# Performance work log

Hardware: AMD Instinct MI355X
Metric: run time of the kernel (lower is better)

Reference implementation:

```python
import jax, jax.numpy as jnp
import numpy as np

P = 512       # input_shape
HD = 256      # hidden_dim
N = 65536     # number of samples
LAM1 = 1.0
LAM3 = 1.0


def setup_inputs() -> dict:
    key = jax.random.key(0)
    ks = jax.random.split(key, 12)
    def lin(kw, kb, out_d, in_d):
        lim = 1.0 / np.sqrt(in_d)
        W = jax.random.uniform(kw, (out_d, in_d), jnp.float32, -lim, lim)
        b = jax.random.uniform(kb, (out_d,), jnp.float32, -lim, lim)
        return W, b
    W1, b1 = lin(ks[0], ks[1], 200, P + HD)
    W12, b12 = lin(ks[2], ks[3], 100, 200)
    W13, b13 = lin(ks[4], ks[5], 100, 100)
    W2, b2 = lin(ks[6], ks[7], P, 100)
    return {
        "input": jax.random.normal(ks[8], (N, P), jnp.float32),
        "h": jax.random.normal(ks[9], (N, HD), jnp.float32),
        "W1": W1, "b1": b1, "W12": W12, "b12": b12,
        "W13": W13, "b13": b13, "W2": W2, "b2": b2,
        "idx0": 0, "idx1": N,
    }


def reference(input, h, W1, b1, W12, b12, W13, b13, W2, b2, idx0, idx1):
    n = input.shape[0]
    hs = h[idx0:idx1]                                   # [N, HD]
    x = jnp.concatenate([input, hs], axis=1)            # [N, P+HD]
    x = jax.nn.relu(x @ W1.T + b1)                      # dropout = identity (eval)
    x = jax.nn.relu(x @ W12.T + b12)
    x = jax.nn.relu(x @ W13.T + b13)
    f_x_h = x @ W2.T + b2                               # [N, P]
    mu = jnp.mean(hs, axis=0)                           # [HD]
    # S = mean_i <h_i, h_i> : vectorized sum-of-squares (replaces Python loop)
    S = jnp.mean(jnp.sum(hs * hs, axis=1))
    part0 = jnp.linalg.norm(f_x_h[:-1] - input[1:]) / (n - 1)
    part1 = LAM1 * jnp.sum(jnp.abs(mu)) / HD
    part2 = LAM1 * jnp.abs(S / HD - 1.0)
    part3 = LAM3 * jnp.mean(jnp.sum(jnp.abs(hs[1:] - hs[:-1]), axis=1)) / HD
    return (f_x_h, part0, part1, part2, part3)
```

## Files before the change

### kernel.cpp

```cpp
#include <hip/hip_runtime.h>

typedef __bf16 bf16;
typedef __bf16 bf16x4 __attribute__((ext_vector_type(4)));
typedef __bf16 bf16x8 __attribute__((ext_vector_type(8)));
typedef float f32x4 __attribute__((ext_vector_type(4)));

#define N_ROWS 65536

#define W1_E   159744
#define W12_E  25088
#define W13_E  14336
#define W2_E   65536
#define WP_TOTAL (W1_E + W12_E + W13_E + W2_E)
#define W12_OFF_B 319488
#define W13_OFF_B 369664
#define W2_OFF_B  398336
#define BP_OFF_BYTES (WP_TOTAL * 2)
#define BP_FLOATS 944
#define ACC_OFF_BYTES (BP_OFF_BYTES + BP_FLOATS * 4)
#define NCOPY 16
#define P0_IDX (NCOPY * 256)
#define S_IDX0 (P0_IDX + 1)
#define P3_IDX0 (S_IDX0 + NCOPY)
#define ACC_FLOATS (P3_IDX0 + NCOPY)

__device__ inline int swz4(int r) { return (r ^ (r >> 2)) & 3; }

__global__ void pack_kernel(const float* __restrict__ W1, const float* __restrict__ b1,
                            const float* __restrict__ W12, const float* __restrict__ b12,
                            const float* __restrict__ W13, const float* __restrict__ b13,
                            const float* __restrict__ W2, const float* __restrict__ b2,
                            bf16* __restrict__ wp, float* __restrict__ bp) {
  int i = blockIdx.x * 256 + threadIdx.x;
  if (i < WP_TOTAL) {
    float v = 0.0f;
    if (i < W1_E) {
      int s = i / 6656, b = i - s * 6656;
      int r = b >> 5, w = b & 31;
      int k = s * 32 + (((w >> 3) ^ swz4(r)) << 3) + (w & 7);
      if (r < 200) v = W1[r * 768 + k];
    } else if (i < W1_E + W12_E) {
      int j = i - W1_E;
      int s = j / 3584, b = j - s * 3584;
      int r = b >> 5, w = b & 31;
      int k = s * 32 + (((w >> 3) ^ swz4(r)) << 3) + (w & 7);
      if (r < 100 && k < 200) v = W12[r * 200 + k];
    } else if (i < W1_E + W12_E + W13_E) {
      int j = i - (W1_E + W12_E);
      int s = j / 3584, b = j - s * 3584;
      int r = b >> 5, w = b & 31;
      int k = s * 32 + (((w >> 3) ^ swz4(r)) << 3) + (w & 7);
      if (r < 100 && k < 100) v = W13[r * 100 + k];
    } else {
      int j = i - (W1_E + W12_E + W13_E);
      int g = j >> 14, rest = j & 16383;
      int s = rest >> 12, b = rest & 4095;
      int r = b >> 5, w = b & 31;
      int o = g * 128 + r;
      int k = s * 32 + (((w >> 3) ^ swz4(r)) << 3) + (w & 7);
      if (k < 100) v = W2[o * 100 + k];
    }
    wp[i] = (bf16)v;
  } else {
    int j = i - WP_TOTAL;
    if (j < BP_FLOATS) {
      float v = 0.0f;
      if (j < 208)      { if (j < 200) v = b1[j]; }
      else if (j < 320) { int o = j - 208; if (o < 100) v = b12[o]; }
      else if (j < 432) { int o = j - 320; if (o < 100) v = b13[o]; }
      else              { v = b2[j - 432]; }
      bp[j] = v;
    }
  }
}

#define MFMA(a, b, c) __builtin_amdgcn_mfma_f32_16x16x32_bf16((a), (b), (c), 0, 0, 0)

template<int BYTES>
__device__ inline void stage(const char* __restrict__ src, bf16* __restrict__ dstw, int tid) {
  char* dst = (char*)dstw;
  const int off0 = (tid >> 6) * 1024 + (tid & 63) * 16;
  constexpr int NCH = (BYTES + 4095) / 4096;
#pragma unroll
  for (int j = 0; j < NCH; j++) {
    const int off = j * 4096 + off0;
    if ((BYTES & 4095) == 0 || off < BYTES)
      __builtin_amdgcn_global_load_lds(
          (const __attribute__((address_space(1))) void*)(src + off),
          (__attribute__((address_space(3))) void*)(dst + off),
          16, 0, 0);
  }
}

__global__ __launch_bounds__(256, 2) void mlp_main(
    const float* __restrict__ input, const float* __restrict__ h,
    const bf16* __restrict__ wp, const float* __restrict__ bp,
    float* __restrict__ out, float* __restrict__ acc) {
  __shared__ __align__(16) bf16 acts[4][3712];
  __shared__ __align__(16) bf16 wbuf[2][6656];
  __shared__ float wred[4][3];

  const int tid = threadIdx.x;
  const int lane = tid & 63;
  const int wave = tid >> 6;
  const int c16 = lane & 15;
  const int quad = lane >> 4;
  const int m0 = blockIdx.x * 64 + wave * 16;
  const int qs8 = (quad ^ swz4(c16)) * 8;

  const char* wpb = (const char*)wp;
  const float* b1p  = bp;
  const float* b12p = bp + 208;
  const float* b13p = bp + 320;
  const float* b2p  = bp + 432;

  bf16* actw = &acts[wave][0];
  bf16* aw = actw;

  f32x4 csA = (f32x4){0.f, 0.f, 0.f, 0.f};
  f32x4 csB = (f32x4){0.f, 0.f, 0.f, 0.f};
  float s2loc = 0.0f, p3loc = 0.0f;

  f32x4 acc1[13];
#pragma unroll
  for (int t = 0; t < 13; t++) acc1[t] = (f32x4){0.f, 0.f, 0.f, 0.f};

  f32x4 ar[8];
  auto loadA = [&](int kb) {
#pragma unroll
    for (int i = 0; i < 8; i++) {
      const int row = 2 * i + (lane >> 5);
      const int col = (lane & 31) * 4;
      const float* src = (kb < 4)
          ? (input + (size_t)(m0 + row) * 512 + kb * 128 + col)
          : (h + (size_t)(m0 + row) * 256 + (kb - 4) * 128 + col);
      ar[i] = *(const f32x4*)src;
    }
  };
  auto writeA = [&]() {
    const int kk = (lane & 31) >> 3;
    const int q  = ((lane & 31) >> 1) & 3;
    const int sub = (lane & 1) * 4;
#pragma unroll
    for (int i = 0; i < 8; i++) {
      const int row = 2 * i + (lane >> 5);
      bf16x4 cv;
#pragma unroll
      for (int c = 0; c < 4; c++) cv[c] = (bf16)ar[i][c];
      *(bf16x4*)(aw + kk * 512 + row * 32 + ((q ^ swz4(row)) * 8) + sub) = cv;
    }
  };

  stage<13312>(wpb, wbuf[0], tid);
  loadA(0);

  for (int kb = 0; kb < 6; kb++) {
    writeA();
    if (kb >= 4) {
      f32x4* cs = (kb == 4) ? &csA : &csB;
#pragma unroll
      for (int i = 0; i < 8; i++) {
        f32x4 oth;
#pragma unroll
        for (int c = 0; c < 4; c++) oth[c] = __shfl_xor(ar[i][c], 32);
        *cs += ar[i];
#pragma unroll
        for (int c = 0; c < 4; c++) s2loc += ar[i][c] * ar[i][c];
        if (lane < 32) {
#pragma unroll
          for (int c = 0; c < 4; c++) p3loc += __builtin_fabsf(oth[c] - ar[i][c]);
        } else if (i >= 1) {
#pragma unroll
          for (int c = 0; c < 4; c++) p3loc += __builtin_fabsf(oth[c] - ar[i - 1][c]);
        }
      }
    }
    __syncthreads();
#pragma unroll
    for (int j = 0; j < 4; j++) {
      const int ks = kb * 4 + j;
      if (j == 0 && kb + 1 < 6) loadA(kb + 1);
      if (ks + 1 < 24) stage<13312>(wpb + (ks + 1) * 13312, wbuf[(ks + 1) & 1], tid);
      bf16x8 a = *(const bf16x8*)(aw + j * 512 + c16 * 32 + qs8);
      const bf16* buf = wbuf[ks & 1];
#pragma unroll
      for (int t = 0; t < 13; t++) {
        bf16x8 bb = *(const bf16x8*)(buf + (t * 16 + c16) * 32 + qs8);
        acc1[t] = MFMA(a, bb, acc1[t]);
      }
      __syncthreads();
    }
  }
#pragma unroll
  for (int t = 0; t < 13; t++) {
    const float bias = b1p[t * 16 + c16];
#pragma unroll
    for (int r = 0; r < 4; r++)
      actw[(quad * 4 + r) * 232 + t * 16 + c16] = (bf16)fmaxf(acc1[t][r] + bias, 0.0f);
  }
  for (int idx = lane; idx < 256; idx += 64)
    actw[(idx >> 4) * 232 + 208 + (idx & 15)] = (bf16)0.0f;

  f32x4 acc2[7];
#pragma unroll
  for (int t = 0; t < 7; t++) acc2[t] = (f32x4){0.f, 0.f, 0.f, 0.f};

  stage<7168>(wpb + W12_OFF_B, wbuf[0], tid);
  __syncthreads();
#pragma unroll
  for (int ks = 0; ks < 7; ks++) {
    if (ks + 1 < 7) stage<7168>(wpb + W12_OFF_B + (ks + 1) * 7168, wbuf[(ks + 1) & 1], tid);
    bf16x8 a = *(const bf16x8*)(actw + c16 * 232 + ks * 32 + quad * 8);
    const bf16* buf = wbuf[ks & 1];
#pragma unroll
    for (int t = 0; t < 7; t++) {
      bf16x8 bb = *(const bf16x8*)(buf + (t * 16 + c16) * 32 + qs8);
      acc2[t] = MFMA(a, bb, acc2[t]);
    }
    __syncthreads();
  }
#pragma unroll
  for (int t = 0; t < 7; t++) {
    const float bias = b12p[t * 16 + c16];
#pragma unroll
    for (int r = 0; r < 4; r++)
      actw[(quad * 4 + r) * 136 + t * 16 + c16] = (bf16)fmaxf(acc2[t][r] + bias, 0.0f);
  }
  for (int idx = lane; idx < 256; idx += 64)
    actw[(idx >> 4) * 136 + 112 + (idx & 15)] = (bf16)0.0f;

  f32x4 acc3[7];
#pragma unroll
  for (int t = 0; t < 7; t++) acc3[t] = (f32x4){0.f, 0.f, 0.f, 0.f};

  stage<7168>(wpb + W13_OFF_B, wbuf[0], tid);
  __syncthreads();
#pragma unroll
  for (int ks = 0; ks < 4; ks++) {
    if (ks + 1 < 4) stage<7168>(wpb + W13_OFF_B + (ks + 1) * 7168, wbuf[(ks + 1) & 1], tid);
    bf16x8 a = *(const bf16x8*)(actw + c16 * 136 + ks * 32 + quad * 8);
    const bf16* buf = wbuf[ks & 1];
#pragma unroll
    for (int t = 0; t < 7; t++) {
      bf16x8 bb = *(const bf16x8*)(buf + (t * 16 + c16) * 32 + qs8);
      acc3[t] = MFMA(a, bb, acc3[t]);
    }
    __syncthreads();
  }
#pragma unroll
  for (int t = 0; t < 7; t++) {
    const float bias = b13p[t * 16 + c16];
#pragma unroll
    for (int r = 0; r < 4; r++)
      actw[(quad * 4 + r) * 136 + t * 16 + c16] = (bf16)fmaxf(acc3[t][r] + bias, 0.0f);
  }
  for (int idx = lane; idx < 256; idx += 64)
    actw[(idx >> 4) * 136 + 112 + (idx & 15)] = (bf16)0.0f;

  float p0local = 0.0f;
  for (int g = 0; g < 4; g++) {
    f32x4 acc4[8];
#pragma unroll
    for (int t = 0; t < 8; t++) acc4[t] = (f32x4){0.f, 0.f, 0.f, 0.f};

    const char* Wg = wpb + W2_OFF_B + g * 32768;
    stage<8192>(Wg, wbuf[0], tid);
    __syncthreads();
#pragma unroll
    for (int ks = 0; ks < 4; ks++) {
      if (ks + 1 < 4) stage<8192>(Wg + (ks + 1) * 8192, wbuf[(ks + 1) & 1], tid);
      bf16x8 a = *(const bf16x8*)(actw + c16 * 136 + ks * 32 + quad * 8);
      const bf16* buf = wbuf[ks & 1];
#pragma unroll
      for (int t = 0; t < 8; t++) {
        bf16x8 bb = *(const bf16x8*)(buf + (t * 16 + c16) * 32 + qs8);
        acc4[t] = MFMA(a, bb, acc4[t]);
      }
      __syncthreads();
    }
#pragma unroll
    for (int t = 0; t < 8; t++) {
      const int o = g * 128 + t * 16 + c16;
      const float bias = b2p[o];
#pragma unroll
      for (int r = 0; r < 4; r++) {
        const int grow = m0 + quad * 4 + r;
        float v = acc4[t][r] + bias;
        out[(size_t)grow * 512 + o] = v;
        if (grow < N_ROWS - 1) {
          float d = v - input[(size_t)(grow + 1) * 512 + o];
          p0local += d * d;
        }
      }
    }
  }

  {
    const int p = tid >> 6, cq = tid & 63;
    const int rowA = blockIdx.x * 64 + p * 16 + 15;
    if (rowA + 1 < N_ROWS) {
      f32x4 a = *(const f32x4*)(h + (size_t)rowA * 256 + cq * 4);
      f32x4 b = *(const f32x4*)(h + (size_t)(rowA + 1) * 256 + cq * 4);
#pragma unroll
      for (int c = 0; c < 4; c++) p3loc += __builtin_fabsf(b[c] - a[c]);
    }
  }
#pragma unroll
  for (int c = 0; c < 4; c++) {
    csA[c] += __shfl_xor(csA[c], 32);
    csB[c] += __shfl_xor(csB[c], 32);
  }
  f32x4* hred = (f32x4*)&acts[0][0];
  if (lane < 32) hred[wave * 64 + lane] = csA;
  else           hred[wave * 64 + 32 + (lane & 31)] = csB;
#pragma unroll
  for (int off = 32; off > 0; off >>= 1) {
    p0local += __shfl_down(p0local, off);
    s2loc   += __shfl_down(s2loc, off);
    p3loc   += __shfl_down(p3loc, off);
  }
  if (lane == 0) { wred[wave][0] = p0local; wred[wave][1] = s2loc; wred[wave][2] = p3loc; }
  __syncthreads();
  if (tid < 64) {
    f32x4 tot = hred[tid] + hred[64 + tid] + hred[128 + tid] + hred[192 + tid];
    float* dst = acc + (blockIdx.x & (NCOPY - 1)) * 256 + tid * 4;
    atomicAdd(dst + 0, tot[0]);
    atomicAdd(dst + 1, tot[1]);
    atomicAdd(dst + 2, tot[2]);
    atomicAdd(dst + 3, tot[3]);
  }
  if (tid == 0) {
    atomicAdd(&acc[P0_IDX], wred[0][0] + wred[1][0] + wred[2][0] + wred[3][0]);
    atomicAdd(&acc[S_IDX0 + (blockIdx.x & (NCOPY - 1))], wred[0][1] + wred[1][1] + wred[2][1] + wred[3][1]);
    atomicAdd(&acc[P3_IDX0 + (blockIdx.x & (NCOPY - 1))], wred[0][2] + wred[1][2] + wred[2][2] + wred[3][2]);
  }
}

__global__ void finalize(const float* __restrict__ acc, float* __restrict__ out) {
  __shared__ float red[256];
  const int t = threadIdx.x;
  float s = 0.0f;
#pragma unroll
  for (int j = 0; j < NCOPY; j++) s += acc[j * 256 + t];
  red[t] = fabsf(s);
  __syncthreads();
  for (int st = 128; st > 0; st >>= 1) {
    if (t < st) red[t] += red[t + st];
    __syncthreads();
  }
  if (t == 0) {
    float Ssum = 0.f, Psum = 0.f;
#pragma unroll
    for (int j = 0; j < NCOPY; j++) { Ssum += acc[S_IDX0 + j]; Psum += acc[P3_IDX0 + j]; }
    out[(size_t)N_ROWS * 512 + 0] = sqrtf(acc[P0_IDX]) / 65535.0f;
    out[(size_t)N_ROWS * 512 + 1] = red[0] / 65536.0f / 256.0f;
    out[(size_t)N_ROWS * 512 + 2] = fabsf(Ssum / (65536.0f * 256.0f) - 1.0f);
    out[(size_t)N_ROWS * 512 + 3] = Psum / (65535.0f * 256.0f);
  }
}

extern "C" void kernel_launch(void* const* d_in, const int* in_sizes, int n_in,
                              void* d_out, int out_size, void* d_ws, size_t ws_size,
                              hipStream_t stream) {
  const float* input = (const float*)d_in[0];
  const float* h   = (const float*)d_in[1];
  const float* W1  = (const float*)d_in[2];
  const float* b1  = (const float*)d_in[3];
  const float* W12 = (const float*)d_in[4];
  const float* b12 = (const float*)d_in[5];
  const float* W13 = (const float*)d_in[6];
  const float* b13 = (const float*)d_in[7];
  const float* W2  = (const float*)d_in[8];
  const float* b2  = (const float*)d_in[9];
  float* out = (float*)d_out;

  bf16* wp = (bf16*)d_ws;
  float* bp = (float*)((char*)d_ws + BP_OFF_BYTES);
  float* acc = (float*)((char*)d_ws + ACC_OFF_BYTES);

  hipMemsetAsync(acc, 0, ACC_FLOATS * sizeof(float), stream);
  pack_kernel<<<(WP_TOTAL + BP_FLOATS + 255) / 256, 256, 0, stream>>>(
      W1, b1, W12, b12, W13, b13, W2, b2, wp, bp);
  mlp_main<<<N_ROWS / 64, 256, 0, stream>>>(input, h, wp, bp, out, acc);
  finalize<<<1, 256, 0, stream>>>(acc, out);
}
```

Baseline: 408.5 us.

## Process two 64-row tiles per block to reuse layer-1 weight stages

Each block now handles 128 rows as two 64-row sets, running layer-1 MFMAs for both against each staged W1 slice, so W1 LDS staging is amortized over twice the rows and the grid is halved. Layer-1 A operands are now loaded straight from global fp32 and converted in registers instead of going through the LDS swizzle buffer. The h statistics are computed in interleaved steps, and layers 2-4 run sequentially per row set. This raises register pressure (two sets of 13 accumulators) under launch bounds of 2 blocks per CU, and the direct global A loads may be less coalesced.

```diff
diff --git a/kernel.cpp b/kernel.cpp
--- a/kernel.cpp
+++ b/kernel.cpp
@@ -76,6 +76,15 @@
 
 #define MFMA(a, b, c) __builtin_amdgcn_mfma_f32_16x16x32_bf16((a), (b), (c), 0, 0, 0)
 
+__device__ inline bf16x8 cvt8(const float* __restrict__ p) {
+  f32x4 lo = *(const f32x4*)p;
+  f32x4 hi = *(const f32x4*)(p + 4);
+  bf16x8 r;
+#pragma unroll
+  for (int i = 0; i < 4; i++) { r[i] = (bf16)lo[i]; r[4 + i] = (bf16)hi[i]; }
+  return r;
+}
+
 template<int BYTES>
 __device__ inline void stage(const char* __restrict__ src, bf16* __restrict__ dstw, int tid) {
   char* dst = (char*)dstw;
@@ -105,7 +114,8 @@
   const int wave = tid >> 6;
   const int c16 = lane & 15;
   const int quad = lane >> 4;
-  const int m0 = blockIdx.x * 64 + wave * 16;
+  const int m0A = blockIdx.x * 128 + wave * 16;
+  const int m0B = m0A + 64;
   const int qs8 = (quad ^ swz4(c16)) * 8;
 
   const char* wpb = (const char*)wp;
@@ -115,194 +125,195 @@
   const float* b2p  = bp + 432;
 
   bf16* actw = &acts[wave][0];
-  bf16* aw = actw;
 
   f32x4 csA = (f32x4){0.f, 0.f, 0.f, 0.f};
   f32x4 csB = (f32x4){0.f, 0.f, 0.f, 0.f};
   float s2loc = 0.0f, p3loc = 0.0f;
-
-  f32x4 acc1[13];
-#pragma unroll
-  for (int t = 0; t < 13; t++) acc1[t] = (f32x4){0.f, 0.f, 0.f, 0.f};
+  float p0local = 0.0f;
 
   f32x4 ar[8];
-  auto loadA = [&](int kb) {
+  auto loadH = [&](int base, int half) {
 #pragma unroll
     for (int i = 0; i < 8; i++) {
       const int row = 2 * i + (lane >> 5);
-      const int col = (lane & 31) * 4;
-      const float* src = (kb < 4)
-          ? (input + (size_t)(m0 + row) * 512 + kb * 128 + col)
-          : (h + (size_t)(m0 + row) * 256 + (kb - 4) * 128 + col);
-      ar[i] = *(const f32x4*)src;
+      ar[i] = *(const f32x4*)(h + (size_t)(base + row) * 256 + half * 128 + (lane & 31) * 4);
     }
   };
-  auto writeA = [&]() {
-    const int kk = (lane & 31) >> 3;
-    const int q  = ((lane & 31) >> 1) & 3;
-    const int sub = (lane & 1) * 4;
+  auto statsH = [&](f32x4* cs) {
 #pragma unroll
     for (int i = 0; i < 8; i++) {
-      const int row = 2 * i + (lane >> 5);
-      bf16x4 cv;
-#pragma unroll
-      for (int c = 0; c < 4; c++) cv[c] = (bf16)ar[i][c];
-      *(bf16x4*)(aw + kk * 512 + row * 32 + ((q ^ swz4(row)) * 8) + sub) = cv;
+      f32x4 oth;
+#pragma unroll
+      for (int c = 0; c < 4; c++) oth[c] = __shfl_xor(ar[i][c], 32);
+      *cs += ar[i];
+#pragma unroll
+      for (int c = 0; c < 4; c++) s2loc += ar[i][c] * ar[i][c];
+      if (lane < 32) {
+#pragma unroll
+        for (int c = 0; c < 4; c++) p3loc += __builtin_fabsf(oth[c] - ar[i][c]);
+      } else if (i >= 1) {
+#pragma unroll
+        for (int c = 0; c < 4; c++) p3loc += __builtin_fabsf(oth[c] - ar[i - 1][c]);
+      }
     }
   };
 
+  f32x4 accA[13], accB[13];
+#pragma unroll
+  for (int t = 0; t < 13; t++) {
+    accA[t] = (f32x4){0.f, 0.f, 0.f, 0.f};
+    accB[t] = (f32x4){0.f, 0.f, 0.f, 0.f};
+  }
+
   stage<13312>(wpb, wbuf[0], tid);
-  loadA(0);
-
-  for (int kb = 0; kb < 6; kb++) {
-    writeA();
-    if (kb >= 4) {
-      f32x4* cs = (kb == 4) ? &csA : &csB;
-#pragma unroll
-      for (int i = 0; i < 8; i++) {
-        f32x4 oth;
-#pragma unroll
-        for (int c = 0; c < 4; c++) oth[c] = __shfl_xor(ar[i][c], 32);
-        *cs += ar[i];
-#pragma unroll
-        for (int c = 0; c < 4; c++) s2loc += ar[i][c] * ar[i][c];
-        if (lane < 32) {
-#pragma unroll
-          for (int c = 0; c < 4; c++) p3loc += __builtin_fabsf(oth[c] - ar[i][c]);
-        } else if (i >= 1) {
-#pragma unroll
-          for (int c = 0; c < 4; c++) p3loc += __builtin_fabsf(oth[c] - ar[i - 1][c]);
-        }
-      }
+  __syncthreads();
+
+  const float* aArow = input + (size_t)(m0A + c16) * 512 + quad * 8;
+  const float* aBrow = input + (size_t)(m0B + c16) * 512 + quad * 8;
+  const float* hArow = h + (size_t)(m0A + c16) * 256 + quad * 8;
+  const float* hBrow = h + (size_t)(m0B + c16) * 256 + quad * 8;
+
+  for (int ks = 0; ks < 24; ks++) {
+    if (ks + 1 < 24) stage<13312>(wpb + (ks + 1) * 13312, wbuf[(ks + 1) & 1], tid);
+    if (ks == 15) loadH(m0A, 0);
+    else if (ks == 16) statsH(&csA);
+    else if (ks == 17) loadH(m0A, 1);
+    else if (ks == 18) statsH(&csB);
+    else if (ks == 19) loadH(m0B, 0);
+    else if (ks == 20) statsH(&csA);
+    else if (ks == 21) loadH(m0B, 1);
+    else if (ks == 22) statsH(&csB);
+    const int k0 = ks * 32;
+    bf16x8 aA = (k0 < 512) ? cvt8(aArow + k0) : cvt8(hArow + (k0 - 512));
+    bf16x8 aB = (k0 < 512) ? cvt8(aBrow + k0) : cvt8(hBrow + (k0 - 512));
+    const bf16* buf = wbuf[ks & 1];
+#pragma unroll
+    for (int t = 0; t < 13; t++) {
+      bf16x8 bb = *(const bf16x8*)(buf + (t * 16 + c16) * 32 + qs8);
+      accA[t] = MFMA(aA, bb, accA[t]);
+      accB[t] = MFMA(aB, bb, accB[t]);
     }
     __syncthreads();
-#pragma unroll
-    for (int j = 0; j < 4; j++) {
-      const int ks = kb * 4 + j;
-      if (j == 0 && kb + 1 < 6) loadA(kb + 1);
-      if (ks + 1 < 24) stage<13312>(wpb + (ks + 1) * 13312, wbuf[(ks + 1) & 1], tid);
-      bf16x8 a = *(const bf16x8*)(aw + j * 512 + c16 * 32 + qs8);
+  }
+
+  auto runL234 = [&](f32x4 (&acc1)[13], int m0) {
+#pragma unroll
+    for (int t = 0; t < 13; t++) {
+      const float bias = b1p[t * 16 + c16];
+#pragma unroll
+      for (int r = 0; r < 4; r++)
+        actw[(quad * 4 + r) * 232 + t * 16 + c16] = (bf16)fmaxf(acc1[t][r] + bias, 0.0f);
+    }
+    for (int idx = lane; idx < 256; idx += 64)
+      actw[(idx >> 4) * 232 + 208 + (idx & 15)] = (bf16)0.0f;
+
+    f32x4 acc2[7];
+#pragma unroll
+    for (int t = 0; t < 7; t++) acc2[t] = (f32x4){0.f, 0.f, 0.f, 0.f};
+    stage<7168>(wpb + W12_OFF_B, wbuf[0], tid);
+    __syncthreads();
+#pragma unroll
+    for (int ks = 0; ks < 7; ks++) {
+      if (ks + 1 < 7) stage<7168>(wpb + W12_OFF_B + (ks + 1) * 7168, wbuf[(ks + 1) & 1], tid);
+      bf16x8 a = *(const bf16x8*)(actw + c16 * 232 + ks * 32 + quad * 8);
       const bf16* buf = wbuf[ks & 1];
 #pragma unroll
-      for (int t = 0; t < 13; t++) {
+      for (int t = 0; t < 7; t++) {
         bf16x8 bb = *(const bf16x8*)(buf + (t * 16 + c16) * 32 + qs8);
-        acc1[t] = MFMA(a, bb, acc1[t]);
+        acc2[t] = MFMA(a, bb, acc2[t]);
       }
       __syncthreads();
     }
-  }
-#pragma unroll
-  for (int t = 0; t < 13; t++) {
-    const float bias = b1p[t * 16 + c16];
-#pragma unroll
-    for (int r = 0; r < 4; r++)
-      actw[(quad * 4 + r) * 232 + t * 16 + c16] = (bf16)fmaxf(acc1[t][r] + bias, 0.0f);
-  }
-  for (int idx = lane; idx < 256; idx += 64)
-    actw[(idx >> 4) * 232 + 208 + (idx & 15)] = (bf16)0.0f;
-
-  f32x4 acc2[7];
-#pragma unroll
-  for (int t = 0; t < 7; t++) acc2[t] = (f32x4){0.f, 0.f, 0.f, 0.f};
-
-  stage<7168>(wpb + W12_OFF_B, wbuf[0], tid);
-  __syncthreads();
-#pragma unroll
-  for (int ks = 0; ks < 7; ks++) {
-    if (ks + 1 < 7) stage<7168>(wpb + W12_OFF_B + (ks + 1) * 7168, wbuf[(ks + 1) & 1], tid);
-    bf16x8 a = *(const bf16x8*)(actw + c16 * 232 + ks * 32 + quad * 8);
-    const bf16* buf = wbuf[ks & 1];
 #pragma unroll
     for (int t = 0; t < 7; t++) {
-      bf16x8 bb = *(const bf16x8*)(buf + (t * 16 + c16) * 32 + qs8);
-      acc2[t] = MFMA(a, bb, acc2[t]);
-    }
+      const float bias = b12p[t * 16 + c16];
+#pragma unroll
+      for (int r = 0; r < 4; r++)
+        actw[(quad * 4 + r) * 136 + t * 16 + c16] = (bf16)fmaxf(acc2[t][r] + bias, 0.0f);
+    }
+    for (int idx = lane; idx < 256; idx += 64)
+      actw[(idx >> 4) * 136 + 112 + (idx & 15)] = (bf16)0.0f;
+
+    f32x4 acc3[7];
+#pragma unroll
+    for (int t = 0; t < 7; t++) acc3[t] = (f32x4){0.f, 0.f, 0.f, 0.f};
+    stage<7168>(wpb + W13_OFF_B, wbuf[0], tid);
     __syncthreads();
-  }
-#pragma unroll
-  for (int t = 0; t < 7; t++) {
-    const float bias = b12p[t * 16 + c16];
-#pragma unroll
-    for (int r = 0; r < 4; r++)
-      actw[(quad * 4 + r) * 136 + t * 16 + c16] = (bf16)fmaxf(acc2[t][r] + bias, 0.0f);
-  }
-  for (int idx = lane; idx < 256; idx += 64)
-    actw[(idx >> 4) * 136 + 112 + (idx & 15)] = (bf16)0.0f;
-
-  f32x4 acc3[7];
-#pragma unroll
-  for (int t = 0; t < 7; t++) acc3[t] = (f32x4){0.f, 0.f, 0.f, 0.f};
-
-  stage<7168>(wpb + W13_OFF_B, wbuf[0], tid);
-  __syncthreads();
-#pragma unroll
-  for (int ks = 0; ks < 4; ks++) {
-    if (ks + 1 < 4) stage<7168>(wpb + W13_OFF_B + (ks + 1) * 7168, wbuf[(ks + 1) & 1], tid);
-    bf16x8 a = *(const bf16x8*)(actw + c16 * 136 + ks * 32 + quad * 8);
-    const bf16* buf = wbuf[ks & 1];
-#pragma unroll
-    for (int t = 0; t < 7; t++) {
-      bf16x8 bb = *(const bf16x8*)(buf + (t * 16 + c16) * 32 + qs8);
-      acc3[t] = MFMA(a, bb, acc3[t]);
-    }
-    __syncthreads();
-  }
-#pragma unroll
-  for (int t = 0; t < 7; t++) {
-    const float bias = b13p[t * 16 + c16];
-#pragma unroll
-    for (int r = 0; r < 4; r++)
-      actw[(quad * 4 + r) * 136 + t * 16 + c16] = (bf16)fmaxf(acc3[t][r] + bias, 0.0f);
-  }
-  for (int idx = lane; idx < 256; idx += 64)
-    actw[(idx >> 4) * 136 + 112 + (idx & 15)] = (bf16)0.0f;
-
-  float p0local = 0.0f;
-  for (int g = 0; g < 4; g++) {
-    f32x4 acc4[8];
-#pragma unroll
-    for (int t = 0; t < 8; t++) acc4[t] = (f32x4){0.f, 0.f, 0.f, 0.f};
-
-    const char* Wg = wpb + W2_OFF_B + g * 32768;
-    stage<8192>(Wg, wbuf[0], tid);
-    __syncthreads();
 #pragma unroll
     for (int ks = 0; ks < 4; ks++) {
-      if (ks + 1 < 4) stage<8192>(Wg + (ks + 1) * 8192, wbuf[(ks + 1) & 1], tid);
+      if (ks + 1 < 4) stage<7168>(wpb + W13_OFF_B + (ks + 1) * 7168, wbuf[(ks + 1) & 1], tid);
       bf16x8 a = *(const bf16x8*)(actw + c16 * 136 + ks * 32 + quad * 8);
       const bf16* buf = wbuf[ks & 1];
 #pragma unroll
+      for (int t = 0; t < 7; t++) {
+        bf16x8 bb = *(const bf16x8*)(buf + (t * 16 + c16) * 32 + qs8);
+        acc3[t] = MFMA(a, bb, acc3[t]);
+      }
+      __syncthreads();
+    }
+#pragma unroll
+    for (int t = 0; t < 7; t++) {
+      const float bias = b13p[t * 16 + c16];
+#pragma unroll
+      for (int r = 0; r < 4; r++)
+        actw[(quad * 4 + r) * 136 + t * 16 + c16] = (bf16)fmaxf(acc3[t][r] + bias, 0.0f);
+    }
+    for (int idx = lane; idx < 256; idx += 64)
+      actw[(idx >> 4) * 136 + 112 + (idx & 15)] = (bf16)0.0f;
+
+    for (int g = 0; g < 4; g++) {
+      f32x4 acc4[8];
+#pragma unroll
+      for (int t = 0; t < 8; t++) acc4[t] = (f32x4){0.f, 0.f, 0.f, 0.f};
+      const char* Wg = wpb + W2_OFF_B + g * 32768;
+      stage<8192>(Wg, wbuf[0], tid);
+      __syncthreads();
+#pragma unroll
+      for (int ks = 0; ks < 4; ks++) {
+        if (ks + 1 < 4) stage<8192>(Wg + (ks + 1) * 8192, wbuf[(ks + 1) & 1], tid);
+        bf16x8 a = *(const bf16x8*)(actw + c16 * 136 + ks * 32 + quad * 8);
+        const bf16* buf = wbuf[ks & 1];
+#pragma unroll
+        for (int t = 0; t < 8; t++) {
+          bf16x8 bb = *(const bf16x8*)(buf + (t * 16 + c16) * 32 + qs8);
+          acc4[t] = MFMA(a, bb, acc4[t]);
+        }
+        __syncthreads();
+      }
+#pragma unroll
       for (int t = 0; t < 8; t++) {
-        bf16x8 bb = *(const bf16x8*)(buf + (t * 16 + c16) * 32 + qs8);
-        acc4[t] = MFMA(a, bb, acc4[t]);
-      }
-      __syncthreads();
-    }
-#pragma unroll
-    for (int t = 0; t < 8; t++) {
-      const int o = g * 128 + t * 16 + c16;
-      const float bias = b2p[o];
-#pragma unroll
-      for (int r = 0; r < 4; r++) {
-        const int grow = m0 + quad * 4 + r;
-        float v = acc4[t][r] + bias;
-        out[(size_t)grow * 512 + o] = v;
-        if (grow < N_ROWS - 1) {
-          float d = v - input[(size_t)(grow + 1) * 512 + o];
-          p0local += d * d;
+        const int o = g * 128 + t * 16 + c16;
+        const float bias = b2p[o];
+#pragma unroll
+        for (int r = 0; r < 4; r++) {
+          const int grow = m0 + quad * 4 + r;
+          float v = acc4[t][r] + bias;
+          out[(size_t)grow * 512 + o] = v;
+          if (grow < N_ROWS - 1) {
+            float d = v - input[(size_t)(grow + 1) * 512 + o];
+            p0local += d * d;
+          }
         }
       }
     }
-  }
+  };
+
+  runL234(accA, m0A);
+  runL234(accB, m0B);
 
   {
-    const int p = tid >> 6, cq = tid & 63;
-    const int rowA = blockIdx.x * 64 + p * 16 + 15;
+    const int g = tid >> 5, cq = tid & 31;
+    const int rowA = blockIdx.x * 128 + g * 16 + 15;
     if (rowA + 1 < N_ROWS) {
-      f32x4 a = *(const f32x4*)(h + (size_t)rowA * 256 + cq * 4);
-      f32x4 b = *(const f32x4*)(h + (size_t)(rowA + 1) * 256 + cq * 4);
-#pragma unroll
-      for (int c = 0; c < 4; c++) p3loc += __builtin_fabsf(b[c] - a[c]);
+      f32x4 a0 = *(const f32x4*)(h + (size_t)rowA * 256 + cq * 8);
+      f32x4 a1 = *(const f32x4*)(h + (size_t)rowA * 256 + cq * 8 + 4);
+      f32x4 b0 = *(const f32x4*)(h + (size_t)(rowA + 1) * 256 + cq * 8);
+      f32x4 b1 = *(const f32x4*)(h + (size_t)(rowA + 1) * 256 + cq * 8 + 4);
+#pragma unroll
+      for (int c = 0; c < 4; c++) {
+        p3loc += __builtin_fabsf(b0[c] - a0[c]);
+        p3loc += __builtin_fabsf(b1[c] - a1[c]);
+      }
     }
   }
 #pragma unroll
@@ -311,6 +322,7 @@
     csB[c] += __shfl_xor(csB[c], 32);
   }
   f32x4* hred = (f32x4*)&acts[0][0];
+  __syncthreads();
   if (lane < 32) hred[wave * 64 + lane] = csA;
   else           hred[wave * 64 + 32 + (lane & 31)] = csB;
 #pragma unroll
@@ -381,6 +393,6 @@
   hipMemsetAsync(acc, 0, ACC_FLOATS * sizeof(float), stream);
   pack_kernel<<<(WP_TOTAL + BP_FLOATS + 255) / 256, 256, 0, stream>>>(
       W1, b1, W12, b12, W13, b13, W2, b2, wp, bp);
-  mlp_main<<<N_ROWS / 64, 256, 0, stream>>>(input, h, wp, bp, out, acc);
+  mlp_main<<<N_ROWS / 128, 256, 0, stream>>>(input, h, wp, bp, out, acc);
   finalize<<<1, 256, 0, stream>>>(acc, out);
 }
```

Result: slower. 434.5 us (+6.4%).

## Shrink LDS footprint to fit three blocks per CU with split W1 staging

Applied to the files above, without the earlier changes.

Raises launch bounds from 2 to 3 blocks per CU and cuts shared memory by halving each weight staging chunk. Each W1 k-slice is now staged in two parts, 7 and 6 output tiles, so the layer-1 loop runs twice as many steps. Each step issues fewer MFMAs and pays its own barrier. Intermediate activations move to the same swizzled [k-slice][row][32] layout used for the input, so later layers read them with the conflict-avoiding qs8 pattern. The extra occupancy is meant to hide memory latency, at the cost of more syncs and register pressure under the tighter launch bound. An added barrier keeps the reuse of acts for the reduction safe.

```diff
diff --git a/kernel.cpp b/kernel.cpp
--- a/kernel.cpp
+++ b/kernel.cpp
@@ -92,12 +92,12 @@
   }
 }
 
-__global__ __launch_bounds__(256, 2) void mlp_main(
+__global__ __launch_bounds__(256, 3) void mlp_main(
     const float* __restrict__ input, const float* __restrict__ h,
     const bf16* __restrict__ wp, const float* __restrict__ bp,
     float* __restrict__ out, float* __restrict__ acc) {
-  __shared__ __align__(16) bf16 acts[4][3712];
-  __shared__ __align__(16) bf16 wbuf[2][6656];
+  __shared__ __align__(16) bf16 acts[4][3584];
+  __shared__ __align__(16) bf16 wbuf[2][4096];
   __shared__ float wred[4][3];
 
   const int tid = threadIdx.x;
@@ -114,12 +114,13 @@
   const float* b13p = bp + 320;
   const float* b2p  = bp + 432;
 
-  bf16* actw = &acts[wave][0];
-  bf16* aw = actw;
+  bf16* actx = &acts[wave][0];
+  bf16* aw = actx;
 
   f32x4 csA = (f32x4){0.f, 0.f, 0.f, 0.f};
   f32x4 csB = (f32x4){0.f, 0.f, 0.f, 0.f};
   float s2loc = 0.0f, p3loc = 0.0f;
+  float p0local = 0.0f;
 
   f32x4 acc1[13];
 #pragma unroll
@@ -151,7 +152,7 @@
     }
   };
 
-  stage<13312>(wpb, wbuf[0], tid);
+  stage<7168>(wpb, wbuf[0], tid);
   loadA(0);
 
   for (int kb = 0; kb < 6; kb++) {
@@ -176,41 +177,64 @@
       }
     }
     __syncthreads();
-#pragma unroll
-    for (int j = 0; j < 4; j++) {
-      const int ks = kb * 4 + j;
+    bf16x8 a;
+#pragma unroll
+    for (int j = 0; j < 8; j++) {
+      const int m = kb * 8 + j;
       if (j == 0 && kb + 1 < 6) loadA(kb + 1);
-      if (ks + 1 < 24) stage<13312>(wpb + (ks + 1) * 13312, wbuf[(ks + 1) & 1], tid);
-      bf16x8 a = *(const bf16x8*)(aw + j * 512 + c16 * 32 + qs8);
-      const bf16* buf = wbuf[ks & 1];
-#pragma unroll
-      for (int t = 0; t < 13; t++) {
-        bf16x8 bb = *(const bf16x8*)(buf + (t * 16 + c16) * 32 + qs8);
-        acc1[t] = MFMA(a, bb, acc1[t]);
+      const int next = m + 1;
+      if (next < 48) {
+        const int sn = next >> 1;
+        if ((next & 1) == 0) stage<7168>(wpb + sn * 13312, wbuf[next & 1], tid);
+        else                 stage<6144>(wpb + sn * 13312 + 7168, wbuf[next & 1], tid);
+      }
+      const bf16* buf = wbuf[m & 1];
+      if ((j & 1) == 0) {
+        a = *(const bf16x8*)(aw + (j >> 1) * 512 + c16 * 32 + qs8);
+#pragma unroll
+        for (int t = 0; t < 7; t++) {
+          bf16x8 bb = *(const bf16x8*)(buf + (t * 16 + c16) * 32 + qs8);
+          acc1[t] = MFMA(a, bb, acc1[t]);
+        }
+      } else {
+#pragma unroll
+        for (int t = 7; t < 13; t++) {
+          bf16x8 bb = *(const bf16x8*)(buf + ((t - 7) * 16 + c16) * 32 + qs8);
+          acc1[t] = MFMA(a, bb, acc1[t]);
+        }
       }
       __syncthreads();
     }
   }
+
 #pragma unroll
   for (int t = 0; t < 13; t++) {
     const float bias = b1p[t * 16 + c16];
-#pragma unroll
-    for (int r = 0; r < 4; r++)
-      actw[(quad * 4 + r) * 232 + t * 16 + c16] = (bf16)fmaxf(acc1[t][r] + bias, 0.0f);
-  }
-  for (int idx = lane; idx < 256; idx += 64)
-    actw[(idx >> 4) * 232 + 208 + (idx & 15)] = (bf16)0.0f;
+    const int col = t * 16 + c16;
+    const int ks = col >> 5, kk = col & 31;
+    const int q = kk >> 3, e = kk & 7;
+#pragma unroll
+    for (int r = 0; r < 4; r++) {
+      const int row = quad * 4 + r;
+      actx[ks * 512 + row * 32 + ((q ^ swz4(row)) << 3) + e] =
+          (bf16)fmaxf(acc1[t][r] + bias, 0.0f);
+    }
+  }
+  for (int idx = lane; idx < 256; idx += 64) {
+    const int row = idx >> 4, kk = 16 + (idx & 15);
+    const int q = kk >> 3, e = kk & 7;
+    actx[6 * 512 + row * 32 + ((q ^ swz4(row)) << 3) + e] = (bf16)0.0f;
+  }
 
   f32x4 acc2[7];
 #pragma unroll
   for (int t = 0; t < 7; t++) acc2[t] = (f32x4){0.f, 0.f, 0.f, 0.f};
-
   stage<7168>(wpb + W12_OFF_B, wbuf[0], tid);
   __syncthreads();
 #pragma unroll
   for (int ks = 0; ks < 7; ks++) {
     if (ks + 1 < 7) stage<7168>(wpb + W12_OFF_B + (ks + 1) * 7168, wbuf[(ks + 1) & 1], tid);
-    bf16x8 a = *(const bf16x8*)(actw + c16 * 232 + ks * 32 + quad * 8);
+    bf16x8 a = *(const bf16x8*)(actx + ks * 512 + c16 * 32 + qs8);
     const bf16* buf = wbuf[ks & 1];
 #pragma unroll
     for (int t = 0; t < 7; t++) {
@@ -222,23 +246,31 @@
 #pragma unroll
   for (int t = 0; t < 7; t++) {
     const float bias = b12p[t * 16 + c16];
-#pragma unroll
-    for (int r = 0; r < 4; r++)
-      actw[(quad * 4 + r) * 136 + t * 16 + c16] = (bf16)fmaxf(acc2[t][r] + bias, 0.0f);
-  }
-  for (int idx = lane; idx < 256; idx += 64)
-    actw[(idx >> 4) * 136 + 112 + (idx & 15)] = (bf16)0.0f;
+    const int col = t * 16 + c16;
+    const int ks = col >> 5, kk = col & 31;
+    const int q = kk >> 3, e = kk & 7;
+#pragma unroll
+    for (int r = 0; r < 4; r++) {
+      const int row = quad * 4 + r;
+      actx[ks * 512 + row * 32 + ((q ^ swz4(row)) << 3) + e] =
+          (bf16)fmaxf(acc2[t][r] + bias, 0.0f);
+    }
+  }
+  for (int idx = lane; idx < 256; idx += 64) {
+    const int row = idx >> 4, kk = 16 + (idx & 15);
+    const int q = kk >> 3, e = kk & 7;
+    actx[3 * 512 + row * 32 + ((q ^ swz4(row)) << 3) + e] = (bf16)0.0f;
+  }
 
   f32x4 acc3[7];
 #pragma unroll
   for (int t = 0; t < 7; t++) acc3[t] = (f32x4){0.f, 0.f, 0.f, 0.f};
-
   stage<7168>(wpb + W13_OFF_B, wbuf[0], tid);
   __syncthreads();
 #pragma unroll
   for (int ks = 0; ks < 4; ks++) {
     if (ks + 1 < 4) stage<7168>(wpb + W13_OFF_B + (ks + 1) * 7168, wbuf[(ks + 1) & 1], tid);
-    bf16x8 a = *(const bf16x8*)(actw + c16 * 136 + ks * 32 + quad * 8);
+    bf16x8 a = *(const bf16x8*)(actx + ks * 512 + c16 * 32 + qs8);
     const bf16* buf = wbuf[ks & 1];
 #pragma unroll
     for (int t = 0; t < 7; t++) {
@@ -250,26 +282,33 @@
 #pragma unroll
   for (int t = 0; t < 7; t++) {
     const float bias = b13p[t * 16 + c16];
-#pragma unroll
-    for (int r = 0; r < 4; r++)
-      actw[(quad * 4 + r) * 136 + t * 16 + c16] = (bf16)fmaxf(acc3[t][r] + bias, 0.0f);
-  }
-  for (int idx = lane; idx < 256; idx += 64)
-    actw[(idx >> 4) * 136 + 112 + (idx & 15)] = (bf16)0.0f;
-
-  float p0local = 0.0f;
+    const int col = t * 16 + c16;
+    const int ks = col >> 5, kk = col & 31;
+    const int q = kk >> 3, e = kk & 7;
+#pragma unroll
+    for (int r = 0; r < 4; r++) {
+      const int row = quad * 4 + r;
+      actx[ks * 512 + row * 32 + ((q ^ swz4(row)) << 3) + e] =
+          (bf16)fmaxf(acc3[t][r] + bias, 0.0f);
+    }
+  }
+  for (int idx = lane; idx < 256; idx += 64) {
+    const int row = idx >> 4, kk = 16 + (idx & 15);
+    const int q = kk >> 3, e = kk & 7;
+    actx[3 * 512 + row * 32 + ((q ^ swz4(row)) << 3) + e] = (bf16)0.0f;
+  }
+
   for (int g = 0; g < 4; g++) {
     f32x4 acc4[8];
 #pragma unroll
     for (int t = 0; t < 8; t++) acc4[t] = (f32x4){0.f, 0.f, 0.f, 0.f};
-
     const char* Wg = wpb + W2_OFF_B + g * 32768;
     stage<8192>(Wg, wbuf[0], tid);
     __syncthreads();
 #pragma unroll
     for (int ks = 0; ks < 4; ks++) {
       if (ks + 1 < 4) stage<8192>(Wg + (ks + 1) * 8192, wbuf[(ks + 1) & 1], tid);
-      bf16x8 a = *(const bf16x8*)(actw + c16 * 136 + ks * 32 + quad * 8);
+      bf16x8 a = *(const bf16x8*)(actx + ks * 512 + c16 * 32 + qs8);
       const bf16* buf = wbuf[ks & 1];
 #pragma unroll
       for (int t = 0; t < 8; t++) {
@@ -311,6 +350,7 @@
     csB[c] += __shfl_xor(csB[c], 32);
   }
   f32x4* hred = (f32x4*)&acts[0][0];
+  __syncthreads();
   if (lane < 32) hred[wave * 64 + lane] = csA;
   else           hred[wave * 64 + 32 + (lane & 31)] = csB;
 #pragma unroll
```

New measurement: 441.4 us. 8.1% more time.
